# Kernel optimization log

Measured on AMD Instinct MI355X. Metric: run time of the kernel, lower is better.

## Reference

```python
import jax, jax.numpy as jnp
import numpy as np

SEQ_LEN = 4096
HIDDEN = 1024
WINDOW = 64  # window_width D; gaussian std = D/2 (Luong local-p)


def setup_inputs() -> dict:
    key = jax.random.key(0)
    k1, k2, k3, k4 = jax.random.split(key, 4)
    scale = 1.0 / np.sqrt(HIDDEN)
    return {
        "source_hidden_states": jax.random.normal(k1, (16, SEQ_LEN, HIDDEN), jnp.float32),
        "target_hidden_state": jax.random.normal(k2, (16, HIDDEN), jnp.float32),
        "W_p": jax.random.normal(k3, (HIDDEN, HIDDEN), jnp.float32) * scale,
        "b_p": jnp.zeros((HIDDEN,), jnp.float32),
        "v_p": jax.random.normal(k4, (HIDDEN,), jnp.float32) * scale,
        "b_v": jnp.zeros((), jnp.float32),
    }


def reference(source_hidden_states, target_hidden_state, W_p, b_p, v_p, b_v):
    # Luong local-p attention, scaled-dot alignment, many-to-one context.
    B, S, H = source_hidden_states.shape
    t = target_hidden_state[:, None, :]  # [B,1,H]

    # predicted aligned position: p = S * sigmoid(v_p^T tanh(W_p h_t))
    hp = jnp.tanh(t @ W_p + b_p)                      # [B,1,H]
    p = jax.nn.sigmoid(hp @ v_p[:, None] + b_v) * S   # [B,1,1] -> squeeze
    p = p[:, :, 0]                                     # [B,1]

    # scaled dot score: sum_h(source * target) / sqrt(H)
    score = jnp.einsum("bsh,bh->bs", source_hidden_states, target_hidden_state)
    score = score * (1.0 / np.sqrt(float(H)))          # [B,S]
    attn = jax.nn.softmax(score, axis=-1)              # [B,S]

    # gaussian window around predicted position, std = D/2
    pos = jnp.arange(S, dtype=jnp.float32)[None, :]    # [1,S]
    sigma = WINDOW / 2.0
    gauss = jnp.exp(-jnp.square(pos - p) / (2.0 * sigma * sigma))  # [B,S]
    attn = attn * gauss

    # context vector
    context = jnp.einsum("bs,bsh->bh", attn, source_hidden_states)  # [B,H]
    return context
```

## Files before the change

kernel.cpp:

```cpp
#include <hip/hip_runtime.h>
#include <math.h>

#define HID 1024
#define SEQ 4096
#define NB 16
#define CHUNK 64
#define NCHUNK (SEQ / CHUNK)

__global__ __launch_bounds__(256) void kA(const float* __restrict__ tgt,
                                          const float* __restrict__ Wp,
                                          const float* __restrict__ bp,
                                          const float* __restrict__ vp,
                                          double* __restrict__ pPart) {
  __shared__ float tl[HID];
  __shared__ double red[4][64];
  const int b = blockIdx.x;
  const int jseg = blockIdx.y;
  const int j0 = jseg * 64;
  const int tid = threadIdx.x;

  #pragma unroll
  for (int k = 0; k < 4; ++k) tl[tid + k * 256] = tgt[b * HID + tid + k * 256];
  __syncthreads();

  const int jl  = tid & 63;
  const int hp4 = tid >> 6;
  double acc = 0.0;
  const float* wcol = Wp + (size_t)(hp4 * 256) * HID + j0 + jl;
  for (int i = 0; i < 256; ++i) {
    acc += (double)tl[hp4 * 256 + i] * (double)wcol[(size_t)i * HID];
  }
  red[hp4][jl] = acc;
  __syncthreads();

  if (tid < 64) {
    double s = red[0][tid] + red[1][tid] + red[2][tid] + red[3][tid];
    double hpv = tanh(s + (double)bp[j0 + tid]);
    double val = hpv * (double)vp[j0 + tid];
    #pragma unroll
    for (int off = 32; off; off >>= 1) val += __shfl_xor(val, off);
    if (tid == 0) pPart[b * 16 + jseg] = val;
  }
}

__global__ __launch_bounds__(256) void kB(const float* __restrict__ src,
                                          const float* __restrict__ tgt,
                                          const double* __restrict__ pPart,
                                          const float* __restrict__ bv,
                                          float* __restrict__ zPart,
                                          float* __restrict__ ctxPart) {
  const int chunk = blockIdx.x;
  const int b = chunk >> 6;
  const int c = chunk & 63;
  const int s0 = c * CHUNK;
  const int tid = threadIdx.x;
  const int wave = tid >> 6;
  const int lane = tid & 63;

  double lg = (double)bv[0];
  #pragma unroll
  for (int i = 0; i < 16; ++i) lg += pPart[b * 16 + i];
  const float pb = (float)(4096.0 / (1.0 + exp(-lg)));

  float4 tf[4];
  const float4* tg4 = (const float4*)(tgt + b * HID);
  #pragma unroll
  for (int k = 0; k < 4; ++k) tf[k] = tg4[k * 64 + lane];

  float4 acc[4];
  #pragma unroll
  for (int k = 0; k < 4; ++k) acc[k] = make_float4(0.f, 0.f, 0.f, 0.f);
  float z = 0.f;

  for (int r = 0; r < 16; ++r) {
    const int s = s0 + wave * 16 + r;
    const float4* srow = (const float4*)(src + ((size_t)b * SEQ + s) * HID);
    float4 x[4];
    #pragma unroll
    for (int k = 0; k < 4; ++k) x[k] = srow[k * 64 + lane];

    float dot = 0.f;
    #pragma unroll
    for (int k = 0; k < 4; ++k) {
      dot = fmaf(x[k].x, tf[k].x, dot);
      dot = fmaf(x[k].y, tf[k].y, dot);
      dot = fmaf(x[k].z, tf[k].z, dot);
      dot = fmaf(x[k].w, tf[k].w, dot);
    }
    #pragma unroll
    for (int off = 32; off; off >>= 1) dot += __shfl_xor(dot, off);

    const float w = expf(dot * 0.03125f);
    const float ds = (float)s - pb;
    const float g = expf(ds * ds * (-1.0f / 2048.0f));
    z += w;
    const float wg = w * g;
    #pragma unroll
    for (int k = 0; k < 4; ++k) {
      acc[k].x = fmaf(wg, x[k].x, acc[k].x);
      acc[k].y = fmaf(wg, x[k].y, acc[k].y);
      acc[k].z = fmaf(wg, x[k].z, acc[k].z);
      acc[k].w = fmaf(wg, x[k].w, acc[k].w);
    }
  }

  __shared__ float lctx[4][HID];
  __shared__ float lz[4];
  #pragma unroll
  for (int k = 0; k < 4; ++k)
    *(float4*)&lctx[wave][k * 256 + lane * 4] = acc[k];
  if (lane == 0) lz[wave] = z;
  __syncthreads();

  float4 s4 = make_float4(0.f, 0.f, 0.f, 0.f);
  #pragma unroll
  for (int w2 = 0; w2 < 4; ++w2) {
    float4 v = *(const float4*)&lctx[w2][tid * 4];
    s4.x += v.x; s4.y += v.y; s4.z += v.z; s4.w += v.w;
  }
  ((float4*)ctxPart)[(size_t)chunk * 256 + tid] = s4;
  if (tid == 0) zPart[chunk] = lz[0] + lz[1] + lz[2] + lz[3];
}

__global__ __launch_bounds__(256) void kC(const float* __restrict__ zPart,
                                          const float* __restrict__ ctxPart,
                                          float* __restrict__ out) {
  const int b = blockIdx.x;
  const int tid = threadIdx.x;
  float Z = 0.f;
  for (int c = 0; c < NCHUNK; ++c) Z += zPart[b * NCHUNK + c];
  const float inv = 1.0f / Z;
  float4 s4 = make_float4(0.f, 0.f, 0.f, 0.f);
  const float4* cp = (const float4*)ctxPart;
  for (int c = 0; c < NCHUNK; ++c) {
    float4 v = cp[((size_t)(b * NCHUNK + c)) * 256 + tid];
    s4.x += v.x; s4.y += v.y; s4.z += v.z; s4.w += v.w;
  }
  ((float4*)out)[b * 256 + tid] =
      make_float4(s4.x * inv, s4.y * inv, s4.z * inv, s4.w * inv);
}

extern "C" void kernel_launch(void* const* d_in, const int* in_sizes, int n_in,
                              void* d_out, int out_size, void* d_ws, size_t ws_size,
                              hipStream_t stream) {
  const float* src = (const float*)d_in[0];
  const float* tgt = (const float*)d_in[1];
  const float* Wp  = (const float*)d_in[2];
  const float* bp  = (const float*)d_in[3];
  const float* vp  = (const float*)d_in[4];
  const float* bv  = (const float*)d_in[5];
  float* out = (float*)d_out;

  double* pPart  = (double*)d_ws;
  float* zPart   = (float*)((char*)d_ws + 4096);
  float* ctxPart = (float*)((char*)d_ws + 8192);

  kA<<<dim3(NB, 16), 256, 0, stream>>>(tgt, Wp, bp, vp, pPart);
  kB<<<NB * NCHUNK, 256, 0, stream>>>(src, tgt, pPart, bv, zPart, ctxPart);
  kC<<<NB, 256, 0, stream>>>(zPart, ctxPart, out);
}
```

Baseline: 72.77 us.

## Double-buffer source row loads with nontemporal loads and split kA accumulators

In the main streaming kernel, the next source row is loaded while the current row is processed (register double-buffering), and the row loop is fully unrolled. Loads use nontemporal hints so the 256MB stream does not pollute cache. The W_p projection kernel splits its double accumulator into four independent chains to shorten the dependency chain. The cost is more register pressure per thread, which may reduce occupancy in a memory-bound kernel.

```diff
diff --git a/kernel.cpp b/kernel.cpp
--- a/kernel.cpp
+++ b/kernel.cpp
@@ -6,6 +6,8 @@
 #define NB 16
 #define CHUNK 64
 #define NCHUNK (SEQ / CHUNK)
+
+typedef float floatx4 __attribute__((ext_vector_type(4)));
 
 __global__ __launch_bounds__(256) void kA(const float* __restrict__ tgt,
                                           const float* __restrict__ Wp,
@@ -25,12 +27,16 @@
 
   const int jl  = tid & 63;
   const int hp4 = tid >> 6;
-  double acc = 0.0;
+  double a0 = 0.0, a1 = 0.0, a2 = 0.0, a3 = 0.0;
   const float* wcol = Wp + (size_t)(hp4 * 256) * HID + j0 + jl;
-  for (int i = 0; i < 256; ++i) {
-    acc += (double)tl[hp4 * 256 + i] * (double)wcol[(size_t)i * HID];
+  const float* tq = tl + hp4 * 256;
+  for (int i = 0; i < 256; i += 4) {
+    a0 += (double)tq[i + 0] * (double)wcol[(size_t)(i + 0) * HID];
+    a1 += (double)tq[i + 1] * (double)wcol[(size_t)(i + 1) * HID];
+    a2 += (double)tq[i + 2] * (double)wcol[(size_t)(i + 2) * HID];
+    a3 += (double)tq[i + 3] * (double)wcol[(size_t)(i + 3) * HID];
   }
-  red[hp4][jl] = acc;
+  red[hp4][jl] = (a0 + a1) + (a2 + a3);
   __syncthreads();
 
   if (tid < 64) {
@@ -41,6 +47,11 @@
     for (int off = 32; off; off >>= 1) val += __shfl_xor(val, off);
     if (tid == 0) pPart[b * 16 + jseg] = val;
   }
+}
+
+__device__ __forceinline__ float4 nt_load4(const float* p) {
+  floatx4 v = __builtin_nontemporal_load((const floatx4*)p);
+  return make_float4(v.x, v.y, v.z, v.w);
 }
 
 __global__ __launch_bounds__(256) void kB(const float* __restrict__ src,
@@ -72,35 +83,44 @@
   for (int k = 0; k < 4; ++k) acc[k] = make_float4(0.f, 0.f, 0.f, 0.f);
   float z = 0.f;
 
+  const int srow0 = s0 + wave * 16;
+  const float* base = src + ((size_t)b * SEQ + srow0) * HID;
+
+  float4 x[2][4];
+  #pragma unroll
+  for (int k = 0; k < 4; ++k) x[0][k] = nt_load4(base + (k * 64 + lane) * 4);
+
+  #pragma unroll
   for (int r = 0; r < 16; ++r) {
-    const int s = s0 + wave * 16 + r;
-    const float4* srow = (const float4*)(src + ((size_t)b * SEQ + s) * HID);
-    float4 x[4];
-    #pragma unroll
-    for (int k = 0; k < 4; ++k) x[k] = srow[k * 64 + lane];
+    const int cur = r & 1, nxt = cur ^ 1;
+    if (r + 1 < 16) {
+      #pragma unroll
+      for (int k = 0; k < 4; ++k)
+        x[nxt][k] = nt_load4(base + ((r + 1) * 256 + k * 64 + lane) * 4);
+    }
 
     float dot = 0.f;
     #pragma unroll
     for (int k = 0; k < 4; ++k) {
-      dot = fmaf(x[k].x, tf[k].x, dot);
-      dot = fmaf(x[k].y, tf[k].y, dot);
-      dot = fmaf(x[k].z, tf[k].z, dot);
-      dot = fmaf(x[k].w, tf[k].w, dot);
+      dot = fmaf(x[cur][k].x, tf[k].x, dot);
+      dot = fmaf(x[cur][k].y, tf[k].y, dot);
+      dot = fmaf(x[cur][k].z, tf[k].z, dot);
+      dot = fmaf(x[cur][k].w, tf[k].w, dot);
     }
     #pragma unroll
     for (int off = 32; off; off >>= 1) dot += __shfl_xor(dot, off);
 
     const float w = expf(dot * 0.03125f);
-    const float ds = (float)s - pb;
+    const float ds = (float)(srow0 + r) - pb;
     const float g = expf(ds * ds * (-1.0f / 2048.0f));
     z += w;
     const float wg = w * g;
     #pragma unroll
     for (int k = 0; k < 4; ++k) {
-      acc[k].x = fmaf(wg, x[k].x, acc[k].x);
-      acc[k].y = fmaf(wg, x[k].y, acc[k].y);
-      acc[k].z = fmaf(wg, x[k].z, acc[k].z);
-      acc[k].w = fmaf(wg, x[k].w, acc[k].w);
+      acc[k].x = fmaf(wg, x[cur][k].x, acc[k].x);
+      acc[k].y = fmaf(wg, x[cur][k].y, acc[k].y);
+      acc[k].z = fmaf(wg, x[cur][k].z, acc[k].z);
+      acc[k].w = fmaf(wg, x[cur][k].w, acc[k].w);
     }
   }
 
```

After: 69.22 us. -4.9%, faster.
